# Kernel optimization log

Hardware: AMD Instinct MI355X
Metric: run time of the kernel (lower is better)

Reference implementation:

```python
import jax, jax.numpy as jnp
import numpy as np

N = 50000
E = 800000
IN_DIM = 128
HID_DIM = 128
OUT_DIM = 128
EPS = 1e-5


def setup_inputs() -> dict:
    key = jax.random.key(0)
    ks = jax.random.split(key, 6)
    x = jax.random.normal(ks[0], (N, IN_DIM), dtype=jnp.float32)
    src = jax.random.randint(ks[1], (E,), 0, N, dtype=jnp.int32)
    dst = jax.random.randint(ks[2], (E,), 0, N, dtype=jnp.int32)
    W1 = jax.random.normal(ks[3], (IN_DIM, HID_DIM), dtype=jnp.float32) / np.sqrt(IN_DIM)
    W2 = jax.random.normal(ks[4], (HID_DIM, OUT_DIM), dtype=jnp.float32) / np.sqrt(HID_DIM)
    return {
        "x": x, "src": src, "dst": dst,
        "W1": W1, "b1": jnp.zeros((HID_DIM,), jnp.float32),
        "gamma1": jnp.ones((HID_DIM,), jnp.float32), "beta1": jnp.zeros((HID_DIM,), jnp.float32),
        "W2": W2, "b2": jnp.zeros((OUT_DIM,), jnp.float32),
        "gamma2": jnp.ones((OUT_DIM,), jnp.float32), "beta2": jnp.zeros((OUT_DIM,), jnp.float32),
    }


def _degrees(src, dst, n):
    ones = jnp.ones(src.shape[0], jnp.float32)
    out_deg = jax.ops.segment_sum(ones, src, num_segments=n)
    in_deg = jax.ops.segment_sum(ones, dst, num_segments=n)
    # DGL norm='both' clamps degree to min 1 before pow(-0.5)
    return jnp.clip(out_deg, 1.0) ** -0.5, jnp.clip(in_deg, 1.0) ** -0.5


def _gconv(h, src, dst, d_out, d_in, W, b):
    h = h * d_out[:, None]                                   # [N, d] src-side norm
    m = jax.ops.segment_sum(h[src], dst, num_segments=h.shape[0])  # SpMM aggregate
    m = m * d_in[:, None]                                    # dst-side norm
    return m @ W + b


def _bn(h, gamma, beta):
    mu = jnp.mean(h, axis=0)
    var = jnp.var(h, axis=0)  # biased, matches torch BN training forward
    return gamma * (h - mu) * jax.lax.rsqrt(var + EPS) + beta


def reference(x, src, dst, W1, b1, gamma1, beta1, W2, b2, gamma2, beta2):
    d_out, d_in = _degrees(src, dst, x.shape[0])
    h1 = jax.nn.relu(_bn(_gconv(x, src, dst, d_out, d_in, W1, b1), gamma1, beta1))
    # dropout is identity in eval mode
    h2 = _bn(_gconv(h1, src, dst, d_out, d_in, W2, b2), gamma2, beta2)
    return jax.nn.relu(h2 + h1)
```

## Files before the change

kernel.cpp:

```cpp
#include <hip/hip_runtime.h>
#include <hip/hip_fp16.h>

#define NODES 50000
#define EDGES 800000
#define DIM 128
#define EPS_BN 1e-5f
#define SCAN_B 1024
#define SCAN_NB ((NODES + SCAN_B - 1) / SCAN_B)
#define GEMM_NB ((NODES + 63) / 64)
#define NCH 64
#define CHE (EDGES / NCH)
#define NR 4
#define RNG (NODES / NR)
#define PRE_NB ((NODES * 16) / 256)
#define TILE_STRIDE 272

typedef _Float16 half8 __attribute__((ext_vector_type(8)));
typedef float floatx4 __attribute__((ext_vector_type(4)));

union H8 { half8 v; __half2 h2[4]; };

__global__ __launch_bounds__(256) void hist_part_kernel(const int* __restrict__ src,
                                                        const int* __restrict__ dst,
                                                        unsigned short* __restrict__ Psrc,
                                                        unsigned short* __restrict__ Pdst) {
    __shared__ int h[RNG];
    int chunk = blockIdx.x & (NCH - 1);
    int range = blockIdx.x >> 6;
    const int* arr = blockIdx.y ? dst : src;
    unsigned short* P = blockIdx.y ? Pdst : Psrc;
    int base = range * RNG;
    for (int i = threadIdx.x; i < RNG; i += 256) h[i] = 0;
    __syncthreads();
    int e0 = chunk * CHE;
    for (int e = e0 + threadIdx.x; e < e0 + CHE; e += 256) {
        unsigned r = (unsigned)(arr[e] - base);
        if (r < (unsigned)RNG) atomicAdd(&h[r], 1);
    }
    __syncthreads();
    for (int i = threadIdx.x; i < RNG; i += 256)
        P[(size_t)chunk * NODES + base + i] = (unsigned short)h[i];
}

__global__ __launch_bounds__(256) void combine_kernel(const unsigned short* __restrict__ Psrc,
                                                      unsigned short* __restrict__ Pdst,
                                                      int* __restrict__ cnt_in,
                                                      float* __restrict__ dn_out,
                                                      float* __restrict__ sdeg,
                                                      float* __restrict__ dn_in) {
    int v = blockIdx.x * 256 + threadIdx.x;
    if (v >= NODES) return;
    int s = 0;
    #pragma unroll 8
    for (int j = 0; j < NCH; ++j) s += Psrc[(size_t)j * NODES + v];
    float fs = (float)max(s, 1);
    dn_out[v] = rsqrtf(fs);
    sdeg[v] = sqrtf(fs);
    int run = 0;
    #pragma unroll 8
    for (int j = 0; j < NCH; ++j) {
        int t = Pdst[(size_t)j * NODES + v];
        Pdst[(size_t)j * NODES + v] = (unsigned short)run;
        run += t;
    }
    cnt_in[v] = run;
    dn_in[v] = rsqrtf((float)max(run, 1));
}

__global__ __launch_bounds__(SCAN_B) void scan_p1_kernel(const int* __restrict__ cnt,
                                                         int* __restrict__ row_ptr,
                                                         int* __restrict__ blk_sums) {
    __shared__ int sm[SCAN_B];
    int t = threadIdx.x;
    int idx = blockIdx.x * SCAN_B + t;
    int v = (idx < NODES) ? cnt[idx] : 0;
    sm[t] = v;
    __syncthreads();
    #pragma unroll
    for (int off = 1; off < SCAN_B; off <<= 1) {
        int u = (t >= off) ? sm[t - off] : 0;
        __syncthreads();
        sm[t] += u;
        __syncthreads();
    }
    if (idx < NODES) row_ptr[idx] = sm[t] - v;
    if (t == SCAN_B - 1) blk_sums[blockIdx.x] = sm[t];
}

__global__ __launch_bounds__(SCAN_B) void scan_p3_kernel(int* __restrict__ row_ptr,
                                                         const int* __restrict__ blk_sums) {
    __shared__ int soff;
    int t = threadIdx.x;
    if (t < 64) {
        int v = (t < blockIdx.x) ? blk_sums[t] : 0;
        #pragma unroll
        for (int off = 32; off > 0; off >>= 1) v += __shfl_xor(v, off);
        if (t == 0) soff = v;
    }
    __syncthreads();
    int idx = blockIdx.x * SCAN_B + t;
    if (idx < NODES) row_ptr[idx] += soff;
    if (idx == 0) row_ptr[NODES] = EDGES;
}

__global__ __launch_bounds__(256) void fill_kernel(const int* __restrict__ src,
                                                   const int* __restrict__ dst,
                                                   const int* __restrict__ row_ptr,
                                                   const unsigned short* __restrict__ Pdst,
                                                   int* __restrict__ csr_src) {
    __shared__ int h[RNG];
    int chunk = blockIdx.x & (NCH - 1);
    int range = blockIdx.x >> 6;
    int base = range * RNG;
    for (int i = threadIdx.x; i < RNG; i += 256) h[i] = 0;
    __syncthreads();
    int e0 = chunk * CHE;
    const unsigned short* Pj = Pdst + (size_t)chunk * NODES;
    for (int e = e0 + threadIdx.x; e < e0 + CHE; e += 256) {
        int d = dst[e];
        unsigned r = (unsigned)(d - base);
        if (r < (unsigned)RNG) {
            int local = atomicAdd(&h[r], 1);
            csr_src[row_ptr[d] + (int)Pj[d] + local] = src[e];
        }
    }
}

__global__ __launch_bounds__(256) void prescale_w2h_kernel(const float* __restrict__ x,
                                                           const float* __restrict__ dn_out,
                                                           __half* __restrict__ hs,
                                                           const float* __restrict__ W1,
                                                           const float* __restrict__ W2,
                                                           __half* __restrict__ WhT1,
                                                           __half* __restrict__ WhT2,
                                                           float* __restrict__ p2a,
                                                           float* __restrict__ p2b) {
    int b = blockIdx.x;
    if (b >= PRE_NB) {
        int b2 = b - PRE_NB;
        int idx = b2 * 256 + threadIdx.x;
        if (b2 < 32) p2a[b2 * 256 + threadIdx.x] = 0.f;
        else if (b2 < 64) p2b[(b2 - 32) * 256 + threadIdx.x] = 0.f;
        const float* W = (idx < 16384) ? W1 : W2;
        __half* D = (idx < 16384) ? WhT1 : WhT2;
        int i = idx & 16383;
        int n = i >> 7;
        int k = i & 127;
        D[i] = __float2half(W[k * DIM + n]);
        return;
    }
    int idx = b * 256 + threadIdx.x;
    int row = idx >> 4;
    int c8 = (idx & 15) * 8;
    float sc = dn_out[row];
    const float* xp = x + (size_t)row * DIM + c8;
    float4 v0 = *(const float4*)xp;
    float4 v1 = *(const float4*)(xp + 4);
    H8 u;
    u.h2[0] = __floats2half2_rn(v0.x * sc, v0.y * sc);
    u.h2[1] = __floats2half2_rn(v0.z * sc, v0.w * sc);
    u.h2[2] = __floats2half2_rn(v1.x * sc, v1.y * sc);
    u.h2[3] = __floats2half2_rn(v1.z * sc, v1.w * sc);
    *(half8*)((char*)hs + ((size_t)row * DIM + c8) * 2) = u.v;
}

__device__ __forceinline__ void acc_h8(half8 raw, float* a) {
    H8 u; u.v = raw;
    #pragma unroll
    for (int k = 0; k < 4; ++k) {
        float2 f = __half22float2(u.h2[k]);
        a[2 * k] += f.x;
        a[2 * k + 1] += f.y;
    }
}

__global__ __launch_bounds__(256) void pullgemm_kernel(const __half* __restrict__ hs,
                                                       const int* __restrict__ row_ptr,
                                                       const int* __restrict__ csr_src,
                                                       const float* __restrict__ dn_in,
                                                       const __half* __restrict__ WhT,
                                                       const float* __restrict__ bias,
                                                       __half* __restrict__ hraw,
                                                       float* __restrict__ p2) {
    __shared__ char smem[64 * TILE_STRIDE];
    int t = threadIdx.x;
    int w = t >> 6;
    int lane = t & 63;
    int q = lane >> 4;
    int c = lane & 15;
    const char* base = (const char*)hs;

    for (int i = 0; i < 16; ++i) {
        int ln = w * 16 + i;
        int node = blockIdx.x * 64 + ln;
        float a[8];
        #pragma unroll
        for (int j = 0; j < 8; ++j) a[j] = 0.f;
        if (node < NODES) {
            int beg = row_ptr[node];
            int end = row_ptr[node + 1];
            int eb = beg;
            for (; eb + 16 <= end; eb += 16) {
                int s0 = csr_src[eb + q];
                int s1 = csr_src[eb + 4 + q];
                int s2 = csr_src[eb + 8 + q];
                int s3 = csr_src[eb + 12 + q];
                half8 v0 = *(const half8*)(base + (size_t)s0 * 256 + c * 16);
                half8 v1 = *(const half8*)(base + (size_t)s1 * 256 + c * 16);
                half8 v2 = *(const half8*)(base + (size_t)s2 * 256 + c * 16);
                half8 v3 = *(const half8*)(base + (size_t)s3 * 256 + c * 16);
                acc_h8(v0, a);
                acc_h8(v1, a);
                acc_h8(v2, a);
                acc_h8(v3, a);
            }
            for (; eb + 8 <= end; eb += 8) {
                int s0 = csr_src[eb + q];
                int s1 = csr_src[eb + 4 + q];
                half8 v0 = *(const half8*)(base + (size_t)s0 * 256 + c * 16);
                half8 v1 = *(const half8*)(base + (size_t)s1 * 256 + c * 16);
                acc_h8(v0, a);
                acc_h8(v1, a);
            }
            for (; eb + 4 <= end; eb += 4) {
                int s0 = csr_src[eb + q];
                half8 v0 = *(const half8*)(base + (size_t)s0 * 256 + c * 16);
                acc_h8(v0, a);
            }
            if (eb + q < end) {
                int s0 = csr_src[eb + q];
                half8 v0 = *(const half8*)(base + (size_t)s0 * 256 + c * 16);
                acc_h8(v0, a);
            }
            #pragma unroll
            for (int j = 0; j < 8; ++j) a[j] += __shfl_xor(a[j], 32);
            #pragma unroll
            for (int j = 0; j < 8; ++j) a[j] += __shfl_xor(a[j], 16);
        }
        if (lane < 16) {
            float sc = (node < NODES) ? dn_in[node] : 0.f;
            H8 u;
            #pragma unroll
            for (int k = 0; k < 4; ++k)
                u.h2[k] = __floats2half2_rn(a[2 * k] * sc, a[2 * k + 1] * sc);
            *(half8*)(smem + ln * TILE_STRIDE + c * 16) = u.v;
        }
    }
    __syncthreads();

    int m = c;
    int quad = q;
    int r0 = blockIdx.x * 64 + w * 16;

    half8 afrag[4];
    #pragma unroll
    for (int kt = 0; kt < 4; ++kt)
        afrag[kt] = *(const half8*)(smem + (w * 16 + m) * TILE_STRIDE + kt * 64 + quad * 16);

    floatx4 acc[8];
    floatx4 zf = {0.f, 0.f, 0.f, 0.f};
    #pragma unroll
    for (int ct = 0; ct < 8; ++ct) acc[ct] = zf;

    #pragma unroll
    for (int kt = 0; kt < 4; ++kt) {
        #pragma unroll
        for (int ct = 0; ct < 8; ++ct) {
            half8 b = *(const half8*)((const char*)WhT + (ct * 16 + m) * 256 + kt * 64 + quad * 16);
            acc[ct] = __builtin_amdgcn_mfma_f32_16x16x32_f16(afrag[kt], b, acc[ct], 0, 0, 0);
        }
    }

    __syncthreads();

    float* ps = (float*)smem;
    int g = w * 4 + quad;
    #pragma unroll
    for (int ct = 0; ct < 8; ++ct) {
        int col = ct * 16 + m;
        float bb = bias[col];
        float cs = 0.f, cq = 0.f;
        #pragma unroll
        for (int reg = 0; reg < 4; ++reg) {
            int row = r0 + quad * 4 + reg;
            if (row < NODES) {
                float o = acc[ct][reg] + bb;
                hraw[(size_t)row * DIM + col] = __float2half(o);
                cs += o;
                cq += o * o;
            }
        }
        ps[g * 128 + col] = cs;
        ps[2048 + g * 128 + col] = cq;
    }
    __syncthreads();

    float* pslot = p2 + (blockIdx.x & 31) * 256;
    if (t < 128) {
        float s = 0.f;
        #pragma unroll
        for (int gg = 0; gg < 16; ++gg) s += ps[gg * 128 + t];
        atomicAdd(pslot + t, s);
    } else {
        int cc = t - 128;
        float s = 0.f;
        #pragma unroll
        for (int gg = 0; gg < 16; ++gg) s += ps[2048 + gg * 128 + cc];
        atomicAdd(pslot + 128 + cc, s);
    }
}

__global__ __launch_bounds__(256) void bn_relu_scale_kernel(const __half* __restrict__ hraw,
                                                            __half* __restrict__ hs,
                                                            const float* __restrict__ p2,
                                                            const float* __restrict__ g,
                                                            const float* __restrict__ be,
                                                            const float* __restrict__ dn_out) {
    __shared__ float sm[256];
    {
        float s = 0.f;
        #pragma unroll
        for (int r = 0; r < 32; ++r) s += p2[r * 256 + threadIdx.x];
        sm[threadIdx.x] = s;
    }
    __syncthreads();
    int idx = blockIdx.x * 256 + threadIdx.x;
    if (idx >= NODES * 16) return;
    int row = idx >> 4;
    int c8 = (idx & 15) * 8;
    const float invN = 1.0f / NODES;
    H8 u;
    u.v = *(const half8*)((const char*)hraw + ((size_t)row * DIM + c8) * 2);
    float o[8];
    #pragma unroll
    for (int k = 0; k < 4; ++k) {
        float2 f = __half22float2(u.h2[k]);
        o[2 * k] = f.x;
        o[2 * k + 1] = f.y;
    }
    #pragma unroll
    for (int j = 0; j < 8; ++j) {
        int cj = c8 + j;
        float mu = sm[cj] * invN;
        float var = sm[128 + cj] * invN - mu * mu;
        float w = g[cj] * rsqrtf(var + EPS_BN);
        o[j] = fmaxf(w * (o[j] - mu) + be[cj], 0.f);
    }
    H8 us;
    float sc = dn_out[row];
    #pragma unroll
    for (int k = 0; k < 4; ++k)
        us.h2[k] = __floats2half2_rn(o[2 * k] * sc, o[2 * k + 1] * sc);
    *(half8*)((char*)hs + ((size_t)row * DIM + c8) * 2) = us.v;
}

__global__ __launch_bounds__(256) void bn_res_relu_kernel(const __half* __restrict__ hraw,
                                                          const __half* __restrict__ hs,
                                                          const float* __restrict__ sdeg,
                                                          float* __restrict__ out,
                                                          const float* __restrict__ p2,
                                                          const float* __restrict__ g,
                                                          const float* __restrict__ be) {
    __shared__ float sm[256];
    {
        float s = 0.f;
        #pragma unroll
        for (int r = 0; r < 32; ++r) s += p2[r * 256 + threadIdx.x];
        sm[threadIdx.x] = s;
    }
    __syncthreads();
    int idx = blockIdx.x * 256 + threadIdx.x;
    if (idx >= NODES * 16) return;
    int row = idx >> 4;
    int c8 = (idx & 15) * 8;
    const float invN = 1.0f / NODES;
    float sd = sdeg[row];
    H8 u, ur;
    u.v = *(const half8*)((const char*)hraw + ((size_t)row * DIM + c8) * 2);
    ur.v = *(const half8*)((const char*)hs + ((size_t)row * DIM + c8) * 2);
    float o[8], r8[8];
    #pragma unroll
    for (int k = 0; k < 4; ++k) {
        float2 f = __half22float2(u.h2[k]);
        float2 fr = __half22float2(ur.h2[k]);
        o[2 * k] = f.x; o[2 * k + 1] = f.y;
        r8[2 * k] = fr.x * sd; r8[2 * k + 1] = fr.y * sd;
    }
    #pragma unroll
    for (int j = 0; j < 8; ++j) {
        int cj = c8 + j;
        float mu = sm[cj] * invN;
        float var = sm[128 + cj] * invN - mu * mu;
        float w = g[cj] * rsqrtf(var + EPS_BN);
        o[j] = fmaxf(w * (o[j] - mu) + be[cj] + r8[j], 0.f);
    }
    float* op = out + (size_t)row * DIM + c8;
    float4 o0 = {o[0], o[1], o[2], o[3]};
    float4 o1 = {o[4], o[5], o[6], o[7]};
    *(float4*)op = o0;
    *(float4*)(op + 4) = o1;
}

extern "C" void kernel_launch(void* const* d_in, const int* in_sizes, int n_in,
                              void* d_out, int out_size, void* d_ws, size_t ws_size,
                              hipStream_t stream) {
    const float* x      = (const float*)d_in[0];
    const int*   src    = (const int*)d_in[1];
    const int*   dst    = (const int*)d_in[2];
    const float* W1     = (const float*)d_in[3];
    const float* b1     = (const float*)d_in[4];
    const float* gamma1 = (const float*)d_in[5];
    const float* beta1  = (const float*)d_in[6];
    const float* W2     = (const float*)d_in[7];
    const float* b2     = (const float*)d_in[8];
    const float* gamma2 = (const float*)d_in[9];
    const float* beta2  = (const float*)d_in[10];
    float* out = (float*)d_out;

    char* wsc = (char*)d_ws;
    int*   cnt_in   = (int*)wsc;                     wsc += NODES * 4;
    float* dn_out   = (float*)wsc;                   wsc += NODES * 4;
    float* sdeg     = (float*)wsc;                   wsc += NODES * 4;
    float* dn_in    = (float*)wsc;                   wsc += NODES * 4;
    int*   row_ptr  = (int*)wsc;                     wsc += (NODES + 1) * 4;
    int*   csr_src  = (int*)wsc;                     wsc += EDGES * 4;
    int*   blk_sums = (int*)wsc;                     wsc += 64 * 4;
    __half* WhT1    = (__half*)wsc;                  wsc += DIM * DIM * 2;
    __half* WhT2    = (__half*)wsc;                  wsc += DIM * DIM * 2;
    float* p2a      = (float*)wsc;                   wsc += 32 * 256 * 4;
    float* p2b      = (float*)wsc;                   wsc += 32 * 256 * 4;
    unsigned short* Psrc = (unsigned short*)wsc;     wsc += (size_t)NCH * NODES * 2;
    unsigned short* Pdst = (unsigned short*)wsc;     wsc += (size_t)NCH * NODES * 2;
    __half* hs      = (__half*)wsc;                  wsc += (size_t)NODES * DIM * 2;
    __half* hraw    = (__half*)wsc;                  wsc += (size_t)NODES * DIM * 2;

    const int T = 256;
    const int grid_e16 = (NODES * 16 + T - 1) / T;

    hist_part_kernel<<<dim3(NR * NCH, 2), T, 0, stream>>>(src, dst, Psrc, Pdst);
    combine_kernel<<<(NODES + T - 1) / T, T, 0, stream>>>(Psrc, Pdst, cnt_in, dn_out, sdeg, dn_in);
    scan_p1_kernel<<<SCAN_NB, SCAN_B, 0, stream>>>(cnt_in, row_ptr, blk_sums);
    scan_p3_kernel<<<SCAN_NB, SCAN_B, 0, stream>>>(row_ptr, blk_sums);
    fill_kernel<<<NR * NCH, T, 0, stream>>>(src, dst, row_ptr, Pdst, csr_src);

    prescale_w2h_kernel<<<PRE_NB + 128, T, 0, stream>>>(x, dn_out, hs, W1, W2, WhT1, WhT2, p2a, p2b);

    pullgemm_kernel<<<GEMM_NB, T, 0, stream>>>(hs, row_ptr, csr_src, dn_in, WhT1, b1, hraw, p2a);
    bn_relu_scale_kernel<<<grid_e16, T, 0, stream>>>(hraw, hs, p2a, gamma1, beta1, dn_out);

    pullgemm_kernel<<<GEMM_NB, T, 0, stream>>>(hs, row_ptr, csr_src, dn_in, WhT2, b2, hraw, p2b);
    bn_res_relu_kernel<<<grid_e16, T, 0, stream>>>(hraw, hs, sdeg, out, p2b, gamma2, beta2);
}
```

Before: 313.6 us.

## Split fused pull-GEMM into per-node gather kernel and separate MFMA GEMM

Replaces the fused aggregation+GEMM kernel, where each wave serially gathered 16 nodes, with a pull kernel that assigns one node per wave over many more blocks, followed by a standalone MFMA GEMM that reads the aggregated rows from a new global buffer. The GEMM now stages the transposed weight in LDS with padded stride. This aims to raise occupancy and memory-level parallelism in the gather, at the cost of an extra global write and read of the aggregated feature matrix and an additional launch per layer.

After: 275.8 us. 1.14x faster.

```diff
diff --git a/kernel.cpp b/kernel.cpp
--- a/kernel.cpp
+++ b/kernel.cpp
@@ -13,7 +13,6 @@
 #define NR 4
 #define RNG (NODES / NR)
 #define PRE_NB ((NODES * 16) / 256)
-#define TILE_STRIDE 272
 
 typedef _Float16 half8 __attribute__((ext_vector_type(8)));
 typedef float floatx4 __attribute__((ext_vector_type(4)));
@@ -174,106 +173,129 @@
     }
 }
 
-__global__ __launch_bounds__(256) void pullgemm_kernel(const __half* __restrict__ hs,
-                                                       const int* __restrict__ row_ptr,
-                                                       const int* __restrict__ csr_src,
-                                                       const float* __restrict__ dn_in,
-                                                       const __half* __restrict__ WhT,
-                                                       const float* __restrict__ bias,
-                                                       __half* __restrict__ hraw,
-                                                       float* __restrict__ p2) {
-    __shared__ char smem[64 * TILE_STRIDE];
-    int t = threadIdx.x;
-    int w = t >> 6;
-    int lane = t & 63;
+__global__ __launch_bounds__(256) void pull_kernel(const __half* __restrict__ hs,
+                                                   const int* __restrict__ row_ptr,
+                                                   const int* __restrict__ csr_src,
+                                                   const float* __restrict__ dn_in,
+                                                   __half* __restrict__ agg) {
+    int wid = threadIdx.x >> 6;
+    int node = blockIdx.x * 4 + wid;
+    if (node >= NODES) return;
+    int lane = threadIdx.x & 63;
     int q = lane >> 4;
     int c = lane & 15;
     const char* base = (const char*)hs;
-
-    for (int i = 0; i < 16; ++i) {
-        int ln = w * 16 + i;
-        int node = blockIdx.x * 64 + ln;
-        float a[8];
-        #pragma unroll
-        for (int j = 0; j < 8; ++j) a[j] = 0.f;
-        if (node < NODES) {
-            int beg = row_ptr[node];
-            int end = row_ptr[node + 1];
-            int eb = beg;
-            for (; eb + 16 <= end; eb += 16) {
-                int s0 = csr_src[eb + q];
-                int s1 = csr_src[eb + 4 + q];
-                int s2 = csr_src[eb + 8 + q];
-                int s3 = csr_src[eb + 12 + q];
-                half8 v0 = *(const half8*)(base + (size_t)s0 * 256 + c * 16);
-                half8 v1 = *(const half8*)(base + (size_t)s1 * 256 + c * 16);
-                half8 v2 = *(const half8*)(base + (size_t)s2 * 256 + c * 16);
-                half8 v3 = *(const half8*)(base + (size_t)s3 * 256 + c * 16);
-                acc_h8(v0, a);
-                acc_h8(v1, a);
-                acc_h8(v2, a);
-                acc_h8(v3, a);
-            }
-            for (; eb + 8 <= end; eb += 8) {
-                int s0 = csr_src[eb + q];
-                int s1 = csr_src[eb + 4 + q];
-                half8 v0 = *(const half8*)(base + (size_t)s0 * 256 + c * 16);
-                half8 v1 = *(const half8*)(base + (size_t)s1 * 256 + c * 16);
-                acc_h8(v0, a);
-                acc_h8(v1, a);
-            }
-            for (; eb + 4 <= end; eb += 4) {
-                int s0 = csr_src[eb + q];
-                half8 v0 = *(const half8*)(base + (size_t)s0 * 256 + c * 16);
-                acc_h8(v0, a);
-            }
-            if (eb + q < end) {
-                int s0 = csr_src[eb + q];
-                half8 v0 = *(const half8*)(base + (size_t)s0 * 256 + c * 16);
-                acc_h8(v0, a);
-            }
+    int beg = row_ptr[node];
+    int end = row_ptr[node + 1];
+    float a[8];
+    #pragma unroll
+    for (int i = 0; i < 8; ++i) a[i] = 0.f;
+    int eb = beg;
+    for (; eb + 16 <= end; eb += 16) {
+        int s0 = csr_src[eb + q];
+        int s1 = csr_src[eb + 4 + q];
+        int s2 = csr_src[eb + 8 + q];
+        int s3 = csr_src[eb + 12 + q];
+        half8 v0 = *(const half8*)(base + (size_t)s0 * 256 + c * 16);
+        half8 v1 = *(const half8*)(base + (size_t)s1 * 256 + c * 16);
+        half8 v2 = *(const half8*)(base + (size_t)s2 * 256 + c * 16);
+        half8 v3 = *(const half8*)(base + (size_t)s3 * 256 + c * 16);
+        acc_h8(v0, a);
+        acc_h8(v1, a);
+        acc_h8(v2, a);
+        acc_h8(v3, a);
+    }
+    for (; eb + 8 <= end; eb += 8) {
+        int s0 = csr_src[eb + q];
+        int s1 = csr_src[eb + 4 + q];
+        half8 v0 = *(const half8*)(base + (size_t)s0 * 256 + c * 16);
+        half8 v1 = *(const half8*)(base + (size_t)s1 * 256 + c * 16);
+        acc_h8(v0, a);
+        acc_h8(v1, a);
+    }
+    for (; eb + 4 <= end; eb += 4) {
+        int s0 = csr_src[eb + q];
+        half8 v0 = *(const half8*)(base + (size_t)s0 * 256 + c * 16);
+        acc_h8(v0, a);
+    }
+    if (eb + q < end) {
+        int s0 = csr_src[eb + q];
+        half8 v0 = *(const half8*)(base + (size_t)s0 * 256 + c * 16);
+        acc_h8(v0, a);
+    }
+    #pragma unroll
+    for (int i = 0; i < 8; ++i) a[i] += __shfl_xor(a[i], 32);
+    #pragma unroll
+    for (int i = 0; i < 8; ++i) a[i] += __shfl_xor(a[i], 16);
+    if (lane < 16) {
+        float sc = dn_in[node];
+        H8 u;
+        #pragma unroll
+        for (int k = 0; k < 4; ++k)
+            u.h2[k] = __floats2half2_rn(a[2 * k] * sc, a[2 * k + 1] * sc);
+        *(half8*)((char*)agg + (size_t)node * 256 + c * 16) = u.v;
+    }
+}
+
+__global__ __launch_bounds__(256) void gemm_mfma_kernel(const __half* __restrict__ A,
+                                                        const __half* __restrict__ WhT,
+                                                        const float* __restrict__ bias,
+                                                        __half* __restrict__ hraw,
+                                                        float* __restrict__ p2) {
+    __shared__ float smem[8704];
+    __half* wl = (__half*)smem;
+
+    int t = threadIdx.x;
+
+    #pragma unroll
+    for (int i = 0; i < 8; ++i) {
+        int cch = t + 256 * i;
+        int n = cch >> 4;
+        int ch = cch & 15;
+        *(float4*)((char*)wl + n * 272 + ch * 16) =
+            *(const float4*)((const char*)WhT + n * 256 + ch * 16);
+    }
+
+    int w = t >> 6;
+    int lane = t & 63;
+    int m = lane & 15;
+    int quad = lane >> 4;
+    int r0 = blockIdx.x * 64 + w * 16;
+    int arow = r0 + m;
+
+    half8 afrag[4];
+    if (arow < NODES) {
+        const char* ap = (const char*)(A + (size_t)arow * DIM);
+        #pragma unroll
+        for (int kt = 0; kt < 4; ++kt)
+            afrag[kt] = *(const half8*)(ap + kt * 64 + quad * 16);
+    } else {
+        #pragma unroll
+        for (int kt = 0; kt < 4; ++kt)
             #pragma unroll
-            for (int j = 0; j < 8; ++j) a[j] += __shfl_xor(a[j], 32);
-            #pragma unroll
-            for (int j = 0; j < 8; ++j) a[j] += __shfl_xor(a[j], 16);
-        }
-        if (lane < 16) {
-            float sc = (node < NODES) ? dn_in[node] : 0.f;
-            H8 u;
-            #pragma unroll
-            for (int k = 0; k < 4; ++k)
-                u.h2[k] = __floats2half2_rn(a[2 * k] * sc, a[2 * k + 1] * sc);
-            *(half8*)(smem + ln * TILE_STRIDE + c * 16) = u.v;
-        }
-    }
-    __syncthreads();
-
-    int m = c;
-    int quad = q;
-    int r0 = blockIdx.x * 64 + w * 16;
-
-    half8 afrag[4];
-    #pragma unroll
-    for (int kt = 0; kt < 4; ++kt)
-        afrag[kt] = *(const half8*)(smem + (w * 16 + m) * TILE_STRIDE + kt * 64 + quad * 16);
+            for (int j = 0; j < 8; ++j)
+                afrag[kt][j] = (_Float16)0.0f;
+    }
 
     floatx4 acc[8];
     floatx4 zf = {0.f, 0.f, 0.f, 0.f};
     #pragma unroll
     for (int ct = 0; ct < 8; ++ct) acc[ct] = zf;
 
+    __syncthreads();
+
     #pragma unroll
     for (int kt = 0; kt < 4; ++kt) {
         #pragma unroll
         for (int ct = 0; ct < 8; ++ct) {
-            half8 b = *(const half8*)((const char*)WhT + (ct * 16 + m) * 256 + kt * 64 + quad * 16);
+            half8 b = *(const half8*)((const char*)wl + (ct * 16 + m) * 272 + kt * 64 + quad * 16);
             acc[ct] = __builtin_amdgcn_mfma_f32_16x16x32_f16(afrag[kt], b, acc[ct], 0, 0, 0);
         }
     }
 
     __syncthreads();
 
-    float* ps = (float*)smem;
+    float* ps = smem;
     int g = w * 4 + quad;
     #pragma unroll
     for (int ct = 0; ct < 8; ++ct) {
@@ -432,10 +454,12 @@
     unsigned short* Psrc = (unsigned short*)wsc;     wsc += (size_t)NCH * NODES * 2;
     unsigned short* Pdst = (unsigned short*)wsc;     wsc += (size_t)NCH * NODES * 2;
     __half* hs      = (__half*)wsc;                  wsc += (size_t)NODES * DIM * 2;
+    __half* agg     = (__half*)wsc;                  wsc += (size_t)NODES * DIM * 2;
     __half* hraw    = (__half*)wsc;                  wsc += (size_t)NODES * DIM * 2;
 
     const int T = 256;
-    const int grid_e16 = (NODES * 16 + T - 1) / T;
+    const int grid_pull = (NODES + 3) / 4;
+    const int grid_e16  = (NODES * 16 + T - 1) / T;
 
     hist_part_kernel<<<dim3(NR * NCH, 2), T, 0, stream>>>(src, dst, Psrc, Pdst);
     combine_kernel<<<(NODES + T - 1) / T, T, 0, stream>>>(Psrc, Pdst, cnt_in, dn_out, sdeg, dn_in);
@@ -445,9 +469,11 @@
 
     prescale_w2h_kernel<<<PRE_NB + 128, T, 0, stream>>>(x, dn_out, hs, W1, W2, WhT1, WhT2, p2a, p2b);
 
-    pullgemm_kernel<<<GEMM_NB, T, 0, stream>>>(hs, row_ptr, csr_src, dn_in, WhT1, b1, hraw, p2a);
+    pull_kernel<<<grid_pull, T, 0, stream>>>(hs, row_ptr, csr_src, dn_in, agg);
+    gemm_mfma_kernel<<<GEMM_NB, T, 0, stream>>>(agg, WhT1, b1, hraw, p2a);
     bn_relu_scale_kernel<<<grid_e16, T, 0, stream>>>(hraw, hs, p2a, gamma1, beta1, dn_out);
 
-    pullgemm_kernel<<<GEMM_NB, T, 0, stream>>>(hs, row_ptr, csr_src, dn_in, WhT2, b2, hraw, p2b);
+    pull_kernel<<<grid_pull, T, 0, stream>>>(hs, row_ptr, csr_src, dn_in, agg);
+    gemm_mfma_kernel<<<GEMM_NB, T, 0, stream>>>(agg, WhT2, b2, hraw, p2b);
     bn_res_relu_kernel<<<grid_e16, T, 0, stream>>>(hraw, hs, sdeg, out, p2b, gamma2, beta2);
 }
```
